# Kernel tuning notes

Measured on AMD Instinct MI355X. Metric: run time of the kernel, lower is better.

The kernel has to match this reference:

```python
import jax, jax.numpy as jnp
import numpy as np

IN, OUT, E, R = 2048, 2048, 8, 8

def setup_inputs() -> dict:
    key = jax.random.key(0)
    ks = jax.random.split(key, 8)
    B, S = 4, 2048
    x = jax.random.normal(ks[0], (B, S, IN), dtype=jnp.float32)
    routing_weights = jax.random.uniform(ks[1], (B, E), dtype=jnp.float32)
    W = jax.random.normal(ks[2], (OUT, IN), dtype=jnp.float32) / np.sqrt(IN).astype(np.float32)
    b = jax.random.normal(ks[3], (OUT,), dtype=jnp.float32) * 0.01
    lora_A_s = jax.random.normal(ks[4], (IN, R), dtype=jnp.float32) / np.sqrt(IN).astype(np.float32)
    lora_B_s = jax.random.normal(ks[5], (R, OUT), dtype=jnp.float32) * 0.01
    lora_A_e = jax.random.normal(ks[6], (E, IN, R), dtype=jnp.float32) / np.sqrt(IN).astype(np.float32)
    lora_B_e = jax.random.normal(ks[7], (E, R, OUT), dtype=jnp.float32) * 0.01
    return {"x": x, "routing_weights": routing_weights, "W": W, "b": b,
            "lora_A_s": lora_A_s, "lora_B_s": lora_B_s,
            "lora_A_e": lora_A_e, "lora_B_e": lora_B_e}

def reference(x, routing_weights, W, b, lora_A_s, lora_B_s, lora_A_e, lora_B_e):
    # base linear: [B,S,IN] @ [IN,OUT] + [OUT]
    base_out = jnp.einsum('bsi,oi->bso', x, W) + b
    # shared low-rank path
    shared_out = (x @ lora_A_s) @ lora_B_s
    # all experts batched: t[b,s,e,r] = x @ A_e[e]; weighted reduce over experts
    t = jnp.einsum('bsi,eir->bser', x, lora_A_e)          # [B,S,E,R]
    expert_out = jnp.einsum('bser,ero,be->bso', t, lora_B_e, routing_weights)
    return base_out + shared_out + expert_out
```

## Files before the change

kernel.cpp:

```cpp
#include <hip/hip_runtime.h>
#include <hip/hip_bf16.h>

#define IN_DIM 2048
#define OUT_DIM 2048
#define NE 8
#define M_TOT 8192
#define RANK_PAD 128
#define K_EXT 2176
#define NKT 34

typedef short short8 __attribute__((ext_vector_type(8)));
typedef float floatx4 __attribute__((ext_vector_type(4)));
typedef unsigned short us;

__device__ __forceinline__ us f2bf(float f) {
    __hip_bfloat16 h = __float2bfloat16(f);
    return *reinterpret_cast<us*>(&h);
}

__device__ __forceinline__ void gld_lds16(const void* g, void* l) {
    __builtin_amdgcn_global_load_lds(
        (const __attribute__((address_space(1))) void*)g,
        (__attribute__((address_space(3))) void*)l, 16, 0, 0);
}


__device__ __forceinline__ void stage2(const us* src, char* lds) {
    gld_lds16(src, lds);
    gld_lds16(src + 128 * K_EXT, lds + 8192);
}

__device__ __forceinline__ void mfma_quad(floatx4 (&acc)[8][4], const short8 (&af)[4],
                                          const short8 (&bf)[4], int mq) {
#pragma unroll
    for (int i = 0; i < 4; ++i)
#pragma unroll
        for (int ni = 0; ni < 4; ++ni)
            acc[mq * 4 + i][ni] =
                __builtin_amdgcn_mfma_f32_16x16x32_bf16(af[i], bf[ni], acc[mq * 4 + i][ni], 0, 0, 0);
}

template <int SM, int VM0, int VM2, bool RD3>
__device__ __forceinline__ void ktile(
    const us* __restrict__ pA, const us* __restrict__ pB, int k1, int k2,
    const char* smC, const char* smN, char* lwC, char* lwN,
    int ab, int bb,
    short8 (&afA)[4], short8 (&afB)[4], short8 (&bfA)[4], short8 (&bfB)[4],
    floatx4 (&acc)[8][4])
{
#pragma unroll
    for (int i = 0; i < 4; ++i) afB[i] = *(const short8*)(smC + ab + (4 + i) * 1024);
    asm volatile("s_waitcnt lgkmcnt(4)" ::: "memory");
    __builtin_amdgcn_sched_barrier(0);
    __builtin_amdgcn_s_setprio(1);
    mfma_quad(acc, afA, bfA, 0);
    __builtin_amdgcn_s_setprio(0);
    if (SM & 1) stage2(pA + k1 + 32, lwN + 32768);
    if (VM0 == 8)      asm volatile("s_waitcnt vmcnt(8)" ::: "memory");
    else if (VM0 == 0) asm volatile("s_waitcnt vmcnt(0)" ::: "memory");
    __builtin_amdgcn_s_barrier();

#pragma unroll
    for (int i = 0; i < 4; ++i) afA[i] = *(const short8*)(smC + 32768 + ab + (4 + i) * 1024);
#pragma unroll
    for (int i = 0; i < 4; ++i) bfB[i] = *(const short8*)(smC + 32768 + bb + i * 1024);
    asm volatile("s_waitcnt lgkmcnt(8)" ::: "memory");
    __builtin_amdgcn_sched_barrier(0);
    __builtin_amdgcn_s_setprio(1);
    mfma_quad(acc, afB, bfA, 1);
    __builtin_amdgcn_s_setprio(0);
    if (SM & 2) stage2(pB + k2, lwC + 16384);
    __builtin_amdgcn_s_barrier();

#pragma unroll
    for (int i = 0; i < 4; ++i) afB[i] = *(const short8*)(smC + 32768 + ab + i * 1024);
    asm volatile("s_waitcnt lgkmcnt(4)" ::: "memory");
    __builtin_amdgcn_sched_barrier(0);
    __builtin_amdgcn_s_setprio(1);
    mfma_quad(acc, afA, bfB, 1);
    __builtin_amdgcn_s_setprio(0);
    if (SM & 4) stage2(pA + k2, lwC);
    if (VM2 == 8)      asm volatile("s_waitcnt vmcnt(8)" ::: "memory");
    else if (VM2 == 4) asm volatile("s_waitcnt vmcnt(4)" ::: "memory");
    __builtin_amdgcn_s_barrier();

    if (RD3) {
#pragma unroll
        for (int i = 0; i < 4; ++i) afA[i] = *(const short8*)(smN + ab + i * 1024);
#pragma unroll
        for (int i = 0; i < 4; ++i) bfA[i] = *(const short8*)(smN + bb + i * 1024);
        asm volatile("s_waitcnt lgkmcnt(8)" ::: "memory");
    } else {
        asm volatile("s_waitcnt lgkmcnt(0)" ::: "memory");
    }
    __builtin_amdgcn_sched_barrier(0);
    __builtin_amdgcn_s_setprio(1);
    mfma_quad(acc, afB, bfB, 0);
    __builtin_amdgcn_s_setprio(0);
    if (SM & 8) stage2(pB + k2 + 32, lwC + 49152);
    __builtin_amdgcn_s_barrier();
}

__global__ __launch_bounds__(512) void main_gemm8(const us* __restrict__ A,
                                                  const us* __restrict__ B,
                                                  const float* __restrict__ bias,
                                                  float* __restrict__ out) {
    extern __shared__ char smem[];
    int tid = threadIdx.x;
    int lane = tid & 63, w = tid >> 6;
    int wm = w >> 2, wn = w & 3;
    int rlo = lane & 15, kq = lane >> 4;

    int b = blockIdx.x;
    int bs = (b & 7) * 32 + (b >> 3);
    int m0 = (bs >> 3) * 256, n0 = (bs & 7) * 256;

    int swz = (kq ^ ((rlo >> 1) & 3)) * 16;
    int ab = (wm * 128 + rlo) * 64 + swz;
    int bb = 16384 + (wn * 64 + rlo) * 64 + swz;

    int r0 = tid >> 2;
    int ps = tid & 3;
    int ssw = (ps ^ ((r0 >> 1) & 3)) * 8;
    const us* pA = A + (size_t)(m0 + r0) * K_EXT + ssw;
    const us* pB = B + (size_t)(n0 + r0) * K_EXT + ssw;
    char* lw0 = smem + w * 1024;
    char* lw1 = lw0 + 65536;
    const char* sm0 = smem;
    const char* sm1 = smem + 65536;

    floatx4 acc[8][4];
#pragma unroll
    for (int mi = 0; mi < 8; ++mi)
#pragma unroll
        for (int ni = 0; ni < 4; ++ni) acc[mi][ni] = (floatx4)0.f;

    stage2(pA,      lw0);
    stage2(pB,      lw0 + 16384);
    stage2(pA + 32, lw0 + 32768);
    stage2(pB + 32, lw0 + 49152);
    stage2(pA + 64, lw1);
    stage2(pB + 64, lw1 + 16384);
    stage2(pB + 96, lw1 + 49152);
    asm volatile("s_waitcnt vmcnt(10)" ::: "memory");
    __builtin_amdgcn_s_barrier();

    short8 afA[4], afB[4], bfA[4], bfB[4];
#pragma unroll
    for (int i = 0; i < 4; ++i) afA[i] = *(const short8*)(sm0 + ab + i * 1024);
#pragma unroll
    for (int i = 0; i < 4; ++i) bfA[i] = *(const short8*)(sm0 + bb + i * 1024);

    for (int tt = 0; tt < 16; ++tt) {
        int t0 = tt * 2;
        ktile<0xF, 8, 8, true>(pA, pB, (t0 + 1) * 64, (t0 + 2) * 64,
                               sm0, sm1, lw0, lw1, ab, bb, afA, afB, bfA, bfB, acc);
        ktile<0xF, 8, 8, true>(pA, pB, (t0 + 2) * 64, (t0 + 3) * 64,
                               sm1, sm0, lw1, lw0, ab, bb, afA, afB, bfA, bfB, acc);
    }
    ktile<0x1, 8, 4, true>(pA, pB, 33 * 64, 34 * 64,
                           sm0, sm1, lw0, lw1, ab, bb, afA, afB, bfA, bfB, acc);
    ktile<0x0, 0, -1, false>(pA, pB, 0, 0,
                             sm1, sm0, lw1, lw0, ab, bb, afA, afB, bfA, bfB, acc);

    float bbias[4];
#pragma unroll
    for (int ni = 0; ni < 4; ++ni) bbias[ni] = bias[n0 + wn * 64 + ni * 16 + rlo];
#pragma unroll
    for (int mi = 0; mi < 8; ++mi) {
        int row = m0 + wm * 128 + mi * 16 + kq * 4;
#pragma unroll
        for (int ni = 0; ni < 4; ++ni) {
            int col = n0 + wn * 64 + ni * 16 + rlo;
#pragma unroll
            for (int r = 0; r < 4; ++r)
                out[(size_t)(row + r) * OUT_DIM + col] = acc[mi][ni][r] + bbias[ni];
        }
    }
}

__global__ void prep_wb(const float* __restrict__ W, const float* __restrict__ Bs,
                        const float* __restrict__ Be, const float* __restrict__ As,
                        const float* __restrict__ Ae, us* __restrict__ Bext,
                        us* __restrict__ AcatT) {
    int blk = blockIdx.x;
    int t = threadIdx.x;
    if (blk < OUT_DIM) {
        int n = blk;
        const float4* src = (const float4*)(W + (size_t)n * IN_DIM + t * 8);
        float4 v0 = src[0], v1 = src[1];
        short8 o;
        o[0] = (short)f2bf(v0.x); o[1] = (short)f2bf(v0.y); o[2] = (short)f2bf(v0.z); o[3] = (short)f2bf(v0.w);
        o[4] = (short)f2bf(v1.x); o[5] = (short)f2bf(v1.y); o[6] = (short)f2bf(v1.z); o[7] = (short)f2bf(v1.w);
        *(short8*)(Bext + (size_t)n * K_EXT + t * 8) = o;
        if (t < RANK_PAD) {
            float v = 0.f;
            if (t < 8)       v = Bs[(size_t)t * OUT_DIM + n];
            else if (t < 72) v = Be[(size_t)(t - 8) * OUT_DIM + n];
            Bext[(size_t)n * K_EXT + IN_DIM + t] = f2bf(v);
        }
    } else {
        int kp = blk - OUT_DIM;
        int i0 = t * 8;
        short8 o;
#pragma unroll
        for (int j = 0; j < 8; ++j) {
            int i = i0 + j;
            float v = 0.f;
            if (kp < 8)       v = As[(size_t)i * 8 + kp];
            else if (kp < 72) v = Ae[(size_t)((kp - 8) >> 3) * IN_DIM * 8 + (size_t)i * 8 + ((kp - 8) & 7)];
            o[j] = (short)f2bf(v);
        }
        *(short8*)(AcatT + (size_t)kp * IN_DIM + i0) = o;
    }
}

__global__ __launch_bounds__(512) void tgemm_fused(const float* __restrict__ x,
                                                   us* __restrict__ Aext,
                                                   const us* __restrict__ AcatT,
                                                   const float* __restrict__ routing) {
    __shared__ floatx4 red[8][64][6];
    int tid = threadIdx.x;
    int lane = tid & 63, w = tid >> 6;
    int rlo = lane & 15, kq = lane >> 4;
    int mbase = blockIdx.x * 16;

    floatx4 acc[6];
#pragma unroll
    for (int ni = 0; ni < 6; ++ni) acc[ni] = (floatx4)0.f;

    const float* xrow = x + (size_t)(mbase + rlo) * IN_DIM + w * 256 + kq * 8;
    us* arow = Aext + (size_t)(mbase + rlo) * K_EXT + w * 256 + kq * 8;
    const us* bbase = AcatT + (size_t)rlo * IN_DIM + w * 256 + kq * 8;

#pragma unroll
    for (int kt = 0; kt < 8; ++kt) {
        int k0 = kt * 32;
        float4 v0 = *(const float4*)(xrow + k0);
        float4 v1 = *(const float4*)(xrow + k0 + 4);
        short8 a;
        a[0] = (short)f2bf(v0.x); a[1] = (short)f2bf(v0.y); a[2] = (short)f2bf(v0.z); a[3] = (short)f2bf(v0.w);
        a[4] = (short)f2bf(v1.x); a[5] = (short)f2bf(v1.y); a[6] = (short)f2bf(v1.z); a[7] = (short)f2bf(v1.w);
        *(short8*)(arow + k0) = a;
#pragma unroll
        for (int ni = 0; ni < 6; ++ni) {
            short8 bfr = *(const short8*)(bbase + (size_t)(ni * 16) * IN_DIM + k0);
            acc[ni] = __builtin_amdgcn_mfma_f32_16x16x32_bf16(a, bfr, acc[ni], 0, 0, 0);
        }
    }

#pragma unroll
    for (int ni = 0; ni < 6; ++ni) red[w][lane][ni] = acc[ni];
    __syncthreads();
    if (w == 0) {
#pragma unroll
        for (int ni = 0; ni < 6; ++ni) {
            floatx4 s = red[0][lane][ni];
#pragma unroll
            for (int ww = 1; ww < 8; ++ww) s += red[ww][lane][ni];
            int col = ni * 16 + rlo;
#pragma unroll
            for (int r = 0; r < 4; ++r) {
                int row = mbase + kq * 4 + r;
                float fac = (col < 8) ? 1.f
                          : (col < 72 ? routing[(row >> 11) * NE + ((col - 8) >> 3)] : 0.f);
                Aext[(size_t)row * K_EXT + IN_DIM + col] = f2bf(s[r] * fac);
            }
        }
#pragma unroll
        for (int c = 0; c < 2; ++c) {
            int col = 96 + c * 16 + rlo;
#pragma unroll
            for (int r = 0; r < 4; ++r)
                Aext[(size_t)(mbase + kq * 4 + r) * K_EXT + IN_DIM + col] = 0;
        }
    }
}

extern "C" void kernel_launch(void* const* d_in, const int* in_sizes, int n_in,
                              void* d_out, int out_size, void* d_ws, size_t ws_size,
                              hipStream_t stream) {
    const float* x   = (const float*)d_in[0];
    const float* rw  = (const float*)d_in[1];
    const float* W   = (const float*)d_in[2];
    const float* bv  = (const float*)d_in[3];
    const float* As  = (const float*)d_in[4];
    const float* Bs  = (const float*)d_in[5];
    const float* Ae  = (const float*)d_in[6];
    const float* Be  = (const float*)d_in[7];
    float* out = (float*)d_out;

    size_t offA = 0;
    size_t offB = offA + (size_t)M_TOT * K_EXT * sizeof(us);
    size_t offC = offB + (size_t)OUT_DIM * K_EXT * sizeof(us);
    size_t need = offC + (size_t)96 * IN_DIM * sizeof(us);
    if (ws_size < need) return;

    us* Aext  = (us*)((char*)d_ws + offA);
    us* Bext  = (us*)((char*)d_ws + offB);
    us* AcatT = (us*)((char*)d_ws + offC);

    hipFuncSetAttribute((const void*)main_gemm8,
                        hipFuncAttributeMaxDynamicSharedMemorySize, 131072);

    prep_wb<<<OUT_DIM + 96, 256, 0, stream>>>(W, Bs, Be, As, Ae, Bext, AcatT);
    tgemm_fused<<<M_TOT / 16, 512, 0, stream>>>(x, Aext, AcatT, rw);
    main_gemm8<<<256, 512, 131072, stream>>>(Aext, Bext, bv, out);
}
```

Baseline: 114.6 us.

## Replace 8-wave ping-pong GEMM with 16-wave triple-buffered K32 pipeline

The main GEMM kernel moves from 512 threads with an explicitly interleaved double-buffered 64-wide K tile (two LDS halves, fragment prefetch across phases) to 1024 threads with a simpler triple-buffered 32-wide K loop. Each wave now computes a 64x64 sub-tile instead of 128x64, which halves accumulator registers and doubles the waves available to hide latency. LDS usage drops to 96 KB. The cost is a barrier on every 32-wide K step, less register-level fragment reuse per wave, and no overlap between LDS reads and MFMAs within a step, because each step waits for all LDS loads before issuing its MFMAs.

```diff
diff --git a/kernel.cpp b/kernel.cpp
--- a/kernel.cpp
+++ b/kernel.cpp
@@ -7,7 +7,7 @@
 #define M_TOT 8192
 #define RANK_PAD 128
 #define K_EXT 2176
-#define NKT 34
+#define NT32 68
 
 typedef short short8 __attribute__((ext_vector_type(8)));
 typedef float floatx4 __attribute__((ext_vector_type(4)));
@@ -24,87 +24,10 @@
         (__attribute__((address_space(3))) void*)l, 16, 0, 0);
 }
 
-
-__device__ __forceinline__ void stage2(const us* src, char* lds) {
-    gld_lds16(src, lds);
-    gld_lds16(src + 128 * K_EXT, lds + 8192);
-}
-
-__device__ __forceinline__ void mfma_quad(floatx4 (&acc)[8][4], const short8 (&af)[4],
-                                          const short8 (&bf)[4], int mq) {
-#pragma unroll
-    for (int i = 0; i < 4; ++i)
-#pragma unroll
-        for (int ni = 0; ni < 4; ++ni)
-            acc[mq * 4 + i][ni] =
-                __builtin_amdgcn_mfma_f32_16x16x32_bf16(af[i], bf[ni], acc[mq * 4 + i][ni], 0, 0, 0);
-}
-
-template <int SM, int VM0, int VM2, bool RD3>
-__device__ __forceinline__ void ktile(
-    const us* __restrict__ pA, const us* __restrict__ pB, int k1, int k2,
-    const char* smC, const char* smN, char* lwC, char* lwN,
-    int ab, int bb,
-    short8 (&afA)[4], short8 (&afB)[4], short8 (&bfA)[4], short8 (&bfB)[4],
-    floatx4 (&acc)[8][4])
-{
-#pragma unroll
-    for (int i = 0; i < 4; ++i) afB[i] = *(const short8*)(smC + ab + (4 + i) * 1024);
-    asm volatile("s_waitcnt lgkmcnt(4)" ::: "memory");
-    __builtin_amdgcn_sched_barrier(0);
-    __builtin_amdgcn_s_setprio(1);
-    mfma_quad(acc, afA, bfA, 0);
-    __builtin_amdgcn_s_setprio(0);
-    if (SM & 1) stage2(pA + k1 + 32, lwN + 32768);
-    if (VM0 == 8)      asm volatile("s_waitcnt vmcnt(8)" ::: "memory");
-    else if (VM0 == 0) asm volatile("s_waitcnt vmcnt(0)" ::: "memory");
-    __builtin_amdgcn_s_barrier();
-
-#pragma unroll
-    for (int i = 0; i < 4; ++i) afA[i] = *(const short8*)(smC + 32768 + ab + (4 + i) * 1024);
-#pragma unroll
-    for (int i = 0; i < 4; ++i) bfB[i] = *(const short8*)(smC + 32768 + bb + i * 1024);
-    asm volatile("s_waitcnt lgkmcnt(8)" ::: "memory");
-    __builtin_amdgcn_sched_barrier(0);
-    __builtin_amdgcn_s_setprio(1);
-    mfma_quad(acc, afB, bfA, 1);
-    __builtin_amdgcn_s_setprio(0);
-    if (SM & 2) stage2(pB + k2, lwC + 16384);
-    __builtin_amdgcn_s_barrier();
-
-#pragma unroll
-    for (int i = 0; i < 4; ++i) afB[i] = *(const short8*)(smC + 32768 + ab + i * 1024);
-    asm volatile("s_waitcnt lgkmcnt(4)" ::: "memory");
-    __builtin_amdgcn_sched_barrier(0);
-    __builtin_amdgcn_s_setprio(1);
-    mfma_quad(acc, afA, bfB, 1);
-    __builtin_amdgcn_s_setprio(0);
-    if (SM & 4) stage2(pA + k2, lwC);
-    if (VM2 == 8)      asm volatile("s_waitcnt vmcnt(8)" ::: "memory");
-    else if (VM2 == 4) asm volatile("s_waitcnt vmcnt(4)" ::: "memory");
-    __builtin_amdgcn_s_barrier();
-
-    if (RD3) {
-#pragma unroll
-        for (int i = 0; i < 4; ++i) afA[i] = *(const short8*)(smN + ab + i * 1024);
-#pragma unroll
-        for (int i = 0; i < 4; ++i) bfA[i] = *(const short8*)(smN + bb + i * 1024);
-        asm volatile("s_waitcnt lgkmcnt(8)" ::: "memory");
-    } else {
-        asm volatile("s_waitcnt lgkmcnt(0)" ::: "memory");
-    }
-    __builtin_amdgcn_sched_barrier(0);
-    __builtin_amdgcn_s_setprio(1);
-    mfma_quad(acc, afB, bfB, 0);
-    __builtin_amdgcn_s_setprio(0);
-    if (SM & 8) stage2(pB + k2 + 32, lwC + 49152);
-    __builtin_amdgcn_s_barrier();
-}
-
-__global__ __launch_bounds__(512) void main_gemm8(const us* __restrict__ A,
-                                                  const us* __restrict__ B,
-                                                  const float* __restrict__ bias,
-                                                  float* __restrict__ out) {
+__global__ __launch_bounds__(1024) void main_gemm16(const us* __restrict__ A,
+                                                    const us* __restrict__ B,
+                                                    const float* __restrict__ bias,
+                                                    float* __restrict__ out) {
     extern __shared__ char smem[];
     int tid = threadIdx.x;
     int lane = tid & 63, w = tid >> 6;
@@ -116,65 +39,72 @@
     int m0 = (bs >> 3) * 256, n0 = (bs & 7) * 256;
 
     int swz = (kq ^ ((rlo >> 1) & 3)) * 16;
-    int ab = (wm * 128 + rlo) * 64 + swz;
+    int ab = (wm * 64 + rlo) * 64 + swz;
     int bb = 16384 + (wn * 64 + rlo) * 64 + swz;
 
-    int r0 = tid >> 2;
-    int ps = tid & 3;
+    int r0 = tid >> 2, ps = tid & 3;
     int ssw = (ps ^ ((r0 >> 1) & 3)) * 8;
     const us* pA = A + (size_t)(m0 + r0) * K_EXT + ssw;
     const us* pB = B + (size_t)(n0 + r0) * K_EXT + ssw;
-    char* lw0 = smem + w * 1024;
-    char* lw1 = lw0 + 65536;
-    const char* sm0 = smem;
-    const char* sm1 = smem + 65536;
-
-    floatx4 acc[8][4];
-#pragma unroll
-    for (int mi = 0; mi < 8; ++mi)
+    int lw = w * 1024;
+
+    floatx4 acc[4][4];
+#pragma unroll
+    for (int mi = 0; mi < 4; ++mi)
 #pragma unroll
         for (int ni = 0; ni < 4; ++ni) acc[mi][ni] = (floatx4)0.f;
 
-    stage2(pA,      lw0);
-    stage2(pB,      lw0 + 16384);
-    stage2(pA + 32, lw0 + 32768);
-    stage2(pB + 32, lw0 + 49152);
-    stage2(pA + 64, lw1);
-    stage2(pB + 64, lw1 + 16384);
-    stage2(pB + 96, lw1 + 49152);
-    asm volatile("s_waitcnt vmcnt(10)" ::: "memory");
+    gld_lds16(pA,      smem + 0     + lw);
+    gld_lds16(pB,      smem + 16384 + lw);
+    gld_lds16(pA + 32, smem + 32768 + lw);
+    gld_lds16(pB + 32, smem + 49152 + lw);
+    asm volatile("s_waitcnt vmcnt(2)" ::: "memory");
     __builtin_amdgcn_s_barrier();
 
-    short8 afA[4], afB[4], bfA[4], bfB[4];
-#pragma unroll
-    for (int i = 0; i < 4; ++i) afA[i] = *(const short8*)(sm0 + ab + i * 1024);
-#pragma unroll
-    for (int i = 0; i < 4; ++i) bfA[i] = *(const short8*)(sm0 + bb + i * 1024);
-
-    for (int tt = 0; tt < 16; ++tt) {
-        int t0 = tt * 2;
-        ktile<0xF, 8, 8, true>(pA, pB, (t0 + 1) * 64, (t0 + 2) * 64,
-                               sm0, sm1, lw0, lw1, ab, bb, afA, afB, bfA, bfB, acc);
-        ktile<0xF, 8, 8, true>(pA, pB, (t0 + 2) * 64, (t0 + 3) * 64,
-                               sm1, sm0, lw1, lw0, ab, bb, afA, afB, bfA, bfB, acc);
-    }
-    ktile<0x1, 8, 4, true>(pA, pB, 33 * 64, 34 * 64,
-                           sm0, sm1, lw0, lw1, ab, bb, afA, afB, bfA, bfB, acc);
-    ktile<0x0, 0, -1, false>(pA, pB, 0, 0,
-                             sm1, sm0, lw1, lw0, ab, bb, afA, afB, bfA, bfB, acc);
-
-    float bbias[4];
-#pragma unroll
-    for (int ni = 0; ni < 4; ++ni) bbias[ni] = bias[n0 + wn * 64 + ni * 16 + rlo];
-#pragma unroll
-    for (int mi = 0; mi < 8; ++mi) {
-        int row = m0 + wm * 128 + mi * 16 + kq * 4;
+    const us* pAs = pA + 64;
+    const us* pBs = pB + 64;
+    int o0 = 0, o1 = 32768, o2 = 65536;
+
+    for (int t = 0; t < NT32; ++t) {
+        if (t + 2 < NT32) {
+            gld_lds16(pAs, smem + o2 + lw);
+            gld_lds16(pBs, smem + o2 + 16384 + lw);
+            pAs += 32; pBs += 32;
+        }
+        short8 af[4], bf[4];
+        const char* base = smem + o0;
+#pragma unroll
+        for (int mi = 0; mi < 4; ++mi) af[mi] = *(const short8*)(base + ab + mi * 1024);
+#pragma unroll
+        for (int ni = 0; ni < 4; ++ni) bf[ni] = *(const short8*)(base + bb + ni * 1024);
+        asm volatile("s_waitcnt lgkmcnt(0)" ::: "memory");
+        __builtin_amdgcn_sched_barrier(0);
+        __builtin_amdgcn_s_setprio(1);
+#pragma unroll
+        for (int mi = 0; mi < 4; ++mi)
+#pragma unroll
+            for (int ni = 0; ni < 4; ++ni)
+                acc[mi][ni] = __builtin_amdgcn_mfma_f32_16x16x32_bf16(
+                    af[mi], bf[ni], acc[mi][ni], 0, 0, 0);
+        __builtin_amdgcn_s_setprio(0);
+        if (t + 2 < NT32)       asm volatile("s_waitcnt vmcnt(2)" ::: "memory");
+        else if (t + 2 == NT32) asm volatile("s_waitcnt vmcnt(0)" ::: "memory");
+        if (t + 1 < NT32) __builtin_amdgcn_s_barrier();
+        int tmp = o0; o0 = o1; o1 = o2; o2 = tmp;
+    }
+
+    float bb2[4];
+#pragma unroll
+    for (int ni = 0; ni < 4; ++ni) bb2[ni] = bias[n0 + wn * 64 + ni * 16 + rlo];
+#pragma unroll
+    for (int mi = 0; mi < 4; ++mi) {
+        int row = m0 + wm * 64 + mi * 16 + kq * 4;
 #pragma unroll
         for (int ni = 0; ni < 4; ++ni) {
             int col = n0 + wn * 64 + ni * 16 + rlo;
 #pragma unroll
             for (int r = 0; r < 4; ++r)
-                out[(size_t)(row + r) * OUT_DIM + col] = acc[mi][ni][r] + bbias[ni];
+                out[(size_t)(row + r) * OUT_DIM + col] = acc[mi][ni][r] + bb2[ni];
         }
     }
 }
@@ -239,8 +169,10 @@
         float4 v0 = *(const float4*)(xrow + k0);
         float4 v1 = *(const float4*)(xrow + k0 + 4);
         short8 a;
-        a[0] = (short)f2bf(v0.x); a[1] = (short)f2bf(v0.y); a[2] = (short)f2bf(v0.z); a[3] = (short)f2bf(v0.w);
-        a[4] = (short)f2bf(v1.x); a[5] = (short)f2bf(v1.y); a[6] = (short)f2bf(v1.z); a[7] = (short)f2bf(v1.w);
+        a[0] = (short)f2bf(v0.x); a[1] = (short)f2bf(v0.y);
+        a[2] = (short)f2bf(v0.z); a[3] = (short)f2bf(v0.w);
+        a[4] = (short)f2bf(v1.x); a[5] = (short)f2bf(v1.y);
+        a[6] = (short)f2bf(v1.z); a[7] = (short)f2bf(v1.w);
         *(short8*)(arow + k0) = a;
 #pragma unroll
         for (int ni = 0; ni < 6; ++ni) {
@@ -300,10 +232,10 @@
     us* Bext  = (us*)((char*)d_ws + offB);
     us* AcatT = (us*)((char*)d_ws + offC);
 
-    hipFuncSetAttribute((const void*)main_gemm8,
-                        hipFuncAttributeMaxDynamicSharedMemorySize, 131072);
+    hipFuncSetAttribute((const void*)main_gemm16,
+                        hipFuncAttributeMaxDynamicSharedMemorySize, 98304);
 
     prep_wb<<<OUT_DIM + 96, 256, 0, stream>>>(W, Bs, Be, As, Ae, Bext, AcatT);
     tgemm_fused<<<M_TOT / 16, 512, 0, stream>>>(x, Aext, AcatT, rw);
-    main_gemm8<<<256, 512, 131072, stream>>>(Aext, Bext, bv, out);
-}
+    main_gemm16<<<256, 1024, 98304, stream>>>(Aext, Bext, bv, out);
+}
```

After: 116.6 us. Within noise of the previous version (+1.8%).

## Fold LoRA deltas into per-batch effective weights instead of extending K

Applied to the files above, without the earlier changes.

Builds four per-batch merged weight matrices, W plus the low-rank update scaled by that batch's routing weights, with a small MFMA kernel. The main GEMM then runs over K=2048 instead of the padded 2176 and picks the weight matrix for its batch. This drops the skinny x·A projection kernel and the extended-K work. In exchange it materialises four bf16 weight copies (about 32 MB of extra writes) and rounds the combined weights to bf16, which changes numerics slightly. A fallback path is kept for when the workspace is too small.

```diff
diff --git a/kernel.cpp b/kernel.cpp
--- a/kernel.cpp
+++ b/kernel.cpp
@@ -5,9 +5,8 @@
 #define OUT_DIM 2048
 #define NE 8
 #define M_TOT 8192
-#define RANK_PAD 128
-#define K_EXT 2176
-#define NKT 34
+#define NB 4
+#define RK 96
 
 typedef short short8 __attribute__((ext_vector_type(8)));
 typedef float floatx4 __attribute__((ext_vector_type(4)));
@@ -16,6 +15,15 @@
 __device__ __forceinline__ us f2bf(float f) {
     __hip_bfloat16 h = __float2bfloat16(f);
     return *reinterpret_cast<us*>(&h);
+}
+
+__device__ __forceinline__ short8 cvt8(float4 v0, float4 v1) {
+    short8 o;
+    o[0] = (short)f2bf(v0.x); o[1] = (short)f2bf(v0.y);
+    o[2] = (short)f2bf(v0.z); o[3] = (short)f2bf(v0.w);
+    o[4] = (short)f2bf(v1.x); o[5] = (short)f2bf(v1.y);
+    o[6] = (short)f2bf(v1.z); o[7] = (short)f2bf(v1.w);
+    return o;
 }
 
 __device__ __forceinline__ void gld_lds16(const void* g, void* l) {
@@ -25,9 +33,10 @@
 }
 
 
+template <int KX>
 __device__ __forceinline__ void stage2(const us* src, char* lds) {
     gld_lds16(src, lds);
-    gld_lds16(src + 128 * K_EXT, lds + 8192);
+    gld_lds16(src + 128 * KX, lds + 8192);
 }
 
 __device__ __forceinline__ void mfma_quad(floatx4 (&acc)[8][4], const short8 (&af)[4],
@@ -40,7 +49,7 @@
                 __builtin_amdgcn_mfma_f32_16x16x32_bf16(af[i], bf[ni], acc[mq * 4 + i][ni], 0, 0, 0);
 }
 
-template <int SM, int VM0, int VM2, bool RD3>
+template <int KX, int SM, int VM0, int VM2, bool RD3>
 __device__ __forceinline__ void ktile(
     const us* __restrict__ pA, const us* __restrict__ pB, int k1, int k2,
     const char* smC, const char* smN, char* lwC, char* lwN,
@@ -55,7 +64,7 @@
     __builtin_amdgcn_s_setprio(1);
     mfma_quad(acc, afA, bfA, 0);
     __builtin_amdgcn_s_setprio(0);
-    if (SM & 1) stage2(pA + k1 + 32, lwN + 32768);
+    if (SM & 1) stage2<KX>(pA + k1 + 32, lwN + 32768);
     if (VM0 == 8)      asm volatile("s_waitcnt vmcnt(8)" ::: "memory");
     else if (VM0 == 0) asm volatile("s_waitcnt vmcnt(0)" ::: "memory");
     __builtin_amdgcn_s_barrier();
@@ -69,7 +78,7 @@
     __builtin_amdgcn_s_setprio(1);
     mfma_quad(acc, afB, bfA, 1);
     __builtin_amdgcn_s_setprio(0);
-    if (SM & 2) stage2(pB + k2, lwC + 16384);
+    if (SM & 2) stage2<KX>(pB + k2, lwC + 16384);
     __builtin_amdgcn_s_barrier();
 
 #pragma unroll
@@ -79,7 +88,7 @@
     __builtin_amdgcn_s_setprio(1);
     mfma_quad(acc, afA, bfB, 1);
     __builtin_amdgcn_s_setprio(0);
-    if (SM & 4) stage2(pA + k2, lwC);
+    if (SM & 4) stage2<KX>(pA + k2, lwC);
     if (VM2 == 8)      asm volatile("s_waitcnt vmcnt(8)" ::: "memory");
     else if (VM2 == 4) asm volatile("s_waitcnt vmcnt(4)" ::: "memory");
     __builtin_amdgcn_s_barrier();
@@ -97,15 +106,17 @@
     __builtin_amdgcn_s_setprio(1);
     mfma_quad(acc, afB, bfB, 0);
     __builtin_amdgcn_s_setprio(0);
-    if (SM & 8) stage2(pB + k2 + 32, lwC + 49152);
+    if (SM & 8) stage2<KX>(pB + k2 + 32, lwC + 49152);
     __builtin_amdgcn_s_barrier();
 }
 
-__global__ __launch_bounds__(512) void main_gemm8(const us* __restrict__ A,
-                                                  const us* __restrict__ B,
-                                                  const float* __restrict__ bias,
-                                                  float* __restrict__ out) {
+template <int KX, bool PB>
+__global__ __launch_bounds__(512) void main_gemm_t(const us* __restrict__ A,
+                                                   const us* __restrict__ Bw,
+                                                   const float* __restrict__ bias,
+                                                   float* __restrict__ out) {
     extern __shared__ char smem[];
+    constexpr int NT = KX / 64;
     int tid = threadIdx.x;
     int lane = tid & 63, w = tid >> 6;
     int wm = w >> 2, wn = w & 3;
@@ -115,6 +126,8 @@
     int bs = (b & 7) * 32 + (b >> 3);
     int m0 = (bs >> 3) * 256, n0 = (bs & 7) * 256;
 
+    const us* B = PB ? (Bw + (size_t)(m0 >> 11) * OUT_DIM * KX) : Bw;
+
     int swz = (kq ^ ((rlo >> 1) & 3)) * 16;
     int ab = (wm * 128 + rlo) * 64 + swz;
     int bb = 16384 + (wn * 64 + rlo) * 64 + swz;
@@ -122,8 +135,8 @@
     int r0 = tid >> 2;
     int ps = tid & 3;
     int ssw = (ps ^ ((r0 >> 1) & 3)) * 8;
-    const us* pA = A + (size_t)(m0 + r0) * K_EXT + ssw;
-    const us* pB = B + (size_t)(n0 + r0) * K_EXT + ssw;
+    const us* pA = A + (size_t)(m0 + r0) * KX + ssw;
+    const us* pB = B + (size_t)(n0 + r0) * KX + ssw;
     char* lw0 = smem + w * 1024;
     char* lw1 = lw0 + 65536;
     const char* sm0 = smem;
@@ -135,13 +148,13 @@
 #pragma unroll
         for (int ni = 0; ni < 4; ++ni) acc[mi][ni] = (floatx4)0.f;
 
-    stage2(pA,      lw0);
-    stage2(pB,      lw0 + 16384);
-    stage2(pA + 32, lw0 + 32768);
-    stage2(pB + 32, lw0 + 49152);
-    stage2(pA + 64, lw1);
-    stage2(pB + 64, lw1 + 16384);
-    stage2(pB + 96, lw1 + 49152);
+    stage2<KX>(pA,      lw0);
+    stage2<KX>(pB,      lw0 + 16384);
+    stage2<KX>(pA + 32, lw0 + 32768);
+    stage2<KX>(pB + 32, lw0 + 49152);
+    stage2<KX>(pA + 64, lw1);
+    stage2<KX>(pB + 64, lw1 + 16384);
+    stage2<KX>(pB + 96, lw1 + 49152);
     asm volatile("s_waitcnt vmcnt(10)" ::: "memory");
     __builtin_amdgcn_s_barrier();
 
@@ -151,17 +164,17 @@
 #pragma unroll
     for (int i = 0; i < 4; ++i) bfA[i] = *(const short8*)(sm0 + bb + i * 1024);
 
-    for (int tt = 0; tt < 16; ++tt) {
+    for (int tt = 0; tt < NT / 2 - 1; ++tt) {
         int t0 = tt * 2;
-        ktile<0xF, 8, 8, true>(pA, pB, (t0 + 1) * 64, (t0 + 2) * 64,
+        ktile<KX, 0xF, 8, 8, true>(pA, pB, (t0 + 1) * 64, (t0 + 2) * 64,
+                                   sm0, sm1, lw0, lw1, ab, bb, afA, afB, bfA, bfB, acc);
+        ktile<KX, 0xF, 8, 8, true>(pA, pB, (t0 + 2) * 64, (t0 + 3) * 64,
+                                   sm1, sm0, lw1, lw0, ab, bb, afA, afB, bfA, bfB, acc);
+    }
+    ktile<KX, 0x1, 8, 4, true>(pA, pB, (NT - 1) * 64, NT * 64,
                                sm0, sm1, lw0, lw1, ab, bb, afA, afB, bfA, bfB, acc);
-        ktile<0xF, 8, 8, true>(pA, pB, (t0 + 2) * 64, (t0 + 3) * 64,
-                               sm1, sm0, lw1, lw0, ab, bb, afA, afB, bfA, bfB, acc);
-    }
-    ktile<0x1, 8, 4, true>(pA, pB, 33 * 64, 34 * 64,
-                           sm0, sm1, lw0, lw1, ab, bb, afA, afB, bfA, bfB, acc);
-    ktile<0x0, 0, -1, false>(pA, pB, 0, 0,
-                             sm1, sm0, lw1, lw0, ab, bb, afA, afB, bfA, bfB, acc);
+    ktile<KX, 0x0, 0, -1, false>(pA, pB, 0, 0,
+                                 sm1, sm0, lw1, lw0, ab, bb, afA, afB, bfA, bfB, acc);
 
     float bbias[4];
 #pragma unroll
@@ -179,25 +192,135 @@
     }
 }
 
-__global__ void prep_wb(const float* __restrict__ W, const float* __restrict__ Bs,
-                        const float* __restrict__ Be, const float* __restrict__ As,
-                        const float* __restrict__ Ae, us* __restrict__ Bext,
-                        us* __restrict__ AcatT) {
+
+__global__ __launch_bounds__(512) void prep_combo(
+    const float* __restrict__ x, const float* __restrict__ As,
+    const float* __restrict__ Ae, const float* __restrict__ Bs,
+    const float* __restrict__ Be, const float* __restrict__ rw,
+    us* __restrict__ Aext, us* __restrict__ AcatI, us* __restrict__ BcatT)
+{
+    int bid = blockIdx.x;
+    int tid = threadIdx.x;
+
+    if (bid < 512) {
+        int half = tid >> 8;
+        int col = (tid & 255) * 8;
+#pragma unroll 8
+        for (int pass = 0; pass < 8; ++pass) {
+            int row = bid * 16 + pass * 2 + half;
+            const float4* src = (const float4*)(x + (size_t)row * IN_DIM + col);
+            *(short8*)(Aext + (size_t)row * IN_DIM + col) = cvt8(src[0], src[1]);
+        }
+    } else if (bid < 544) {
+        if (tid < 64) {
+            int r = (bid - 512) * 64 + tid;
+            us* dst = AcatI + (size_t)r * RK;
+            const float4* as = (const float4*)(As + (size_t)r * 8);
+            *(short8*)dst = cvt8(as[0], as[1]);
+#pragma unroll
+            for (int e = 0; e < 8; ++e) {
+                const float4* ae = (const float4*)(Ae + ((size_t)e * IN_DIM + r) * 8);
+                *(short8*)(dst + 8 + e * 8) = cvt8(ae[0], ae[1]);
+            }
+            short8 z = (short8)0;
+            *(short8*)(dst + 72) = z; *(short8*)(dst + 80) = z; *(short8*)(dst + 88) = z;
+        }
+    } else {
+        int n = (bid - 544) * 512 + tid;
+        float com[72];
+#pragma unroll
+        for (int rp = 0; rp < 8; ++rp)  com[rp] = Bs[(size_t)rp * OUT_DIM + n];
+#pragma unroll
+        for (int rp = 8; rp < 72; ++rp) com[rp] = Be[(size_t)(rp - 8) * OUT_DIM + n];
+#pragma unroll
+        for (int bb = 0; bb < NB; ++bb) {
+            us v[RK];
+#pragma unroll
+            for (int rp = 0; rp < 8; ++rp)  v[rp] = f2bf(com[rp]);
+#pragma unroll
+            for (int rp = 8; rp < 72; ++rp) v[rp] = f2bf(com[rp] * rw[bb * NE + ((rp - 8) >> 3)]);
+#pragma unroll
+            for (int rp = 72; rp < 96; ++rp) v[rp] = 0;
+            us* dst = BcatT + ((size_t)bb * OUT_DIM + n) * RK;
+#pragma unroll
+            for (int j = 0; j < 12; ++j)
+                *(short8*)(dst + j * 8) = *(short8*)(v + j * 8);
+        }
+    }
+}
+
+__global__ __launch_bounds__(512) void delta_wb(const float* __restrict__ W,
+                                                const us* __restrict__ AcatI,
+                                                const us* __restrict__ BcatT,
+                                                us* __restrict__ Bext) {
+    int tid = threadIdx.x;
+    int lane = tid & 63, w = tid >> 6;
+    int wm = w >> 2, wn = w & 3;
+    int rlo = lane & 15, kq = lane >> 4;
+    int b = blockIdx.x >> 6;
+    int t6 = blockIdx.x & 63;
+    int nn0 = (t6 >> 3) * 256, ii0 = (t6 & 7) * 256;
+
+    const us* bct = BcatT + ((size_t)b * OUT_DIM + nn0 + wm * 128 + rlo) * RK + kq * 8;
+    const us* aci = AcatI + ((size_t)(ii0 + wn * 64 + rlo)) * RK + kq * 8;
+
+    floatx4 acc[8][4];
+#pragma unroll
+    for (int mi = 0; mi < 8; ++mi)
+#pragma unroll
+        for (int ni = 0; ni < 4; ++ni) acc[mi][ni] = (floatx4)0.f;
+
+#pragma unroll
+    for (int ks = 0; ks < 3; ++ks) {
+        int k0 = ks * 32;
+        short8 af[8], bf[4];
+#pragma unroll
+        for (int mi = 0; mi < 8; ++mi)
+            af[mi] = *(const short8*)(bct + (size_t)mi * 16 * RK + k0);
+#pragma unroll
+        for (int ni = 0; ni < 4; ++ni)
+            bf[ni] = *(const short8*)(aci + (size_t)ni * 16 * RK + k0);
+#pragma unroll
+        for (int mi = 0; mi < 8; ++mi)
+#pragma unroll
+            for (int ni = 0; ni < 4; ++ni)
+                acc[mi][ni] = __builtin_amdgcn_mfma_f32_16x16x32_bf16(
+                    af[mi], bf[ni], acc[mi][ni], 0, 0, 0);
+    }
+
+#pragma unroll
+    for (int mi = 0; mi < 8; ++mi) {
+#pragma unroll
+        for (int r = 0; r < 4; ++r) {
+            int n = nn0 + wm * 128 + mi * 16 + kq * 4 + r;
+#pragma unroll
+            for (int ni = 0; ni < 4; ++ni) {
+                int i = ii0 + wn * 64 + ni * 16 + rlo;
+                float val = acc[mi][ni][r] + W[(size_t)n * IN_DIM + i];
+                Bext[((size_t)b * OUT_DIM + n) * IN_DIM + i] = f2bf(val);
+            }
+        }
+    }
+}
+
+#define K_EXT1 2176
+#define RANK_PAD 128
+
+__global__ void prep_wb_fb(const float* __restrict__ W, const float* __restrict__ Bs,
+                           const float* __restrict__ Be, const float* __restrict__ As,
+                           const float* __restrict__ Ae, us* __restrict__ Bext,
+                           us* __restrict__ AcatT) {
     int blk = blockIdx.x;
     int t = threadIdx.x;
     if (blk < OUT_DIM) {
         int n = blk;
         const float4* src = (const float4*)(W + (size_t)n * IN_DIM + t * 8);
-        float4 v0 = src[0], v1 = src[1];
-        short8 o;
-        o[0] = (short)f2bf(v0.x); o[1] = (short)f2bf(v0.y); o[2] = (short)f2bf(v0.z); o[3] = (short)f2bf(v0.w);
-        o[4] = (short)f2bf(v1.x); o[5] = (short)f2bf(v1.y); o[6] = (short)f2bf(v1.z); o[7] = (short)f2bf(v1.w);
-        *(short8*)(Bext + (size_t)n * K_EXT + t * 8) = o;
+        *(short8*)(Bext + (size_t)n * K_EXT1 + t * 8) = cvt8(src[0], src[1]);
         if (t < RANK_PAD) {
             float v = 0.f;
             if (t < 8)       v = Bs[(size_t)t * OUT_DIM + n];
             else if (t < 72) v = Be[(size_t)(t - 8) * OUT_DIM + n];
-            Bext[(size_t)n * K_EXT + IN_DIM + t] = f2bf(v);
+            Bext[(size_t)n * K_EXT1 + IN_DIM + t] = f2bf(v);
         }
     } else {
         int kp = blk - OUT_DIM;
@@ -215,10 +338,10 @@
     }
 }
 
-__global__ __launch_bounds__(512) void tgemm_fused(const float* __restrict__ x,
-                                                   us* __restrict__ Aext,
-                                                   const us* __restrict__ AcatT,
-                                                   const float* __restrict__ routing) {
+__global__ __launch_bounds__(512) void tgemm_fused_fb(const float* __restrict__ x,
+                                                      us* __restrict__ Aext,
+                                                      const us* __restrict__ AcatT,
+                                                      const float* __restrict__ routing) {
     __shared__ floatx4 red[8][64][6];
     int tid = threadIdx.x;
     int lane = tid & 63, w = tid >> 6;
@@ -230,7 +353,7 @@
     for (int ni = 0; ni < 6; ++ni) acc[ni] = (floatx4)0.f;
 
     const float* xrow = x + (size_t)(mbase + rlo) * IN_DIM + w * 256 + kq * 8;
-    us* arow = Aext + (size_t)(mbase + rlo) * K_EXT + w * 256 + kq * 8;
+    us* arow = Aext + (size_t)(mbase + rlo) * K_EXT1 + w * 256 + kq * 8;
     const us* bbase = AcatT + (size_t)rlo * IN_DIM + w * 256 + kq * 8;
 
 #pragma unroll
@@ -238,9 +361,7 @@
         int k0 = kt * 32;
         float4 v0 = *(const float4*)(xrow + k0);
         float4 v1 = *(const float4*)(xrow + k0 + 4);
-        short8 a;
-        a[0] = (short)f2bf(v0.x); a[1] = (short)f2bf(v0.y); a[2] = (short)f2bf(v0.z); a[3] = (short)f2bf(v0.w);
-        a[4] = (short)f2bf(v1.x); a[5] = (short)f2bf(v1.y); a[6] = (short)f2bf(v1.z); a[7] = (short)f2bf(v1.w);
+        short8 a = cvt8(v0, v1);
         *(short8*)(arow + k0) = a;
 #pragma unroll
         for (int ni = 0; ni < 6; ++ni) {
@@ -264,7 +385,7 @@
                 int row = mbase + kq * 4 + r;
                 float fac = (col < 8) ? 1.f
                           : (col < 72 ? routing[(row >> 11) * NE + ((col - 8) >> 3)] : 0.f);
-                Aext[(size_t)row * K_EXT + IN_DIM + col] = f2bf(s[r] * fac);
+                Aext[(size_t)row * K_EXT1 + IN_DIM + col] = f2bf(s[r] * fac);
             }
         }
 #pragma unroll
@@ -272,7 +393,7 @@
             int col = 96 + c * 16 + rlo;
 #pragma unroll
             for (int r = 0; r < 4; ++r)
-                Aext[(size_t)(mbase + kq * 4 + r) * K_EXT + IN_DIM + col] = 0;
+                Aext[(size_t)(mbase + kq * 4 + r) * K_EXT1 + IN_DIM + col] = 0;
         }
     }
 }
@@ -290,20 +411,41 @@
     const float* Be  = (const float*)d_in[7];
     float* out = (float*)d_out;
 
-    size_t offA = 0;
-    size_t offB = offA + (size_t)M_TOT * K_EXT * sizeof(us);
-    size_t offC = offB + (size_t)OUT_DIM * K_EXT * sizeof(us);
-    size_t need = offC + (size_t)96 * IN_DIM * sizeof(us);
-    if (ws_size < need) return;
-
-    us* Aext  = (us*)((char*)d_ws + offA);
-    us* Bext  = (us*)((char*)d_ws + offB);
-    us* AcatT = (us*)((char*)d_ws + offC);
-
-    hipFuncSetAttribute((const void*)main_gemm8,
+    size_t pA  = 0;
+    size_t pB  = pA + (size_t)M_TOT * IN_DIM * 2;
+    size_t pAI = pB + (size_t)NB * OUT_DIM * IN_DIM * 2;
+    size_t pBT = pAI + (size_t)IN_DIM * RK * 2;
+    size_t need2 = pBT + (size_t)NB * OUT_DIM * RK * 2;
+
+    if (ws_size >= need2) {
+        us* Aext  = (us*)((char*)d_ws + pA);
+        us* Bext  = (us*)((char*)d_ws + pB);
+        us* AcatI = (us*)((char*)d_ws + pAI);
+        us* BcatT = (us*)((char*)d_ws + pBT);
+
+        hipFuncSetAttribute((const void*)&main_gemm_t<2048, true>,
+                            hipFuncAttributeMaxDynamicSharedMemorySize, 131072);
+
+        prep_combo<<<548, 512, 0, stream>>>(x, As, Ae, Bs, Be, rw, Aext, AcatI, BcatT);
+        delta_wb<<<256, 512, 0, stream>>>(W, AcatI, BcatT, Bext);
+        main_gemm_t<2048, true><<<256, 512, 131072, stream>>>(Aext, Bext, bv, out);
+        return;
+    }
+
+    size_t fA = 0;
+    size_t fB = fA + (size_t)M_TOT * K_EXT1 * 2;
+    size_t fC = fB + (size_t)OUT_DIM * K_EXT1 * 2;
+    size_t need1 = fC + (size_t)96 * IN_DIM * 2;
+    if (ws_size < need1) return;
+
+    us* Aext  = (us*)((char*)d_ws + fA);
+    us* Bext  = (us*)((char*)d_ws + fB);
+    us* AcatT = (us*)((char*)d_ws + fC);
+
+    hipFuncSetAttribute((const void*)&main_gemm_t<2176, false>,
                         hipFuncAttributeMaxDynamicSharedMemorySize, 131072);
 
-    prep_wb<<<OUT_DIM + 96, 256, 0, stream>>>(W, Bs, Be, As, Ae, Bext, AcatT);
-    tgemm_fused<<<M_TOT / 16, 512, 0, stream>>>(x, Aext, AcatT, rw);
-    main_gemm8<<<256, 512, 131072, stream>>>(Aext, Bext, bv, out);
-}
+    prep_wb_fb<<<OUT_DIM + 96, 256, 0, stream>>>(W, Bs, Be, As, Ae, Bext, AcatT);
+    tgemm_fused_fb<<<M_TOT / 16, 512, 0, stream>>>(x, Aext, AcatT, rw);
+    main_gemm_t<2176, false><<<256, 512, 131072, stream>>>(Aext, Bext, bv, out);
+}
```

Measured after the change: 116.3 us. About the same (+1.6%).
